# Kernel tuning notes

Hardware: AMD Instinct MI355X
Metric: run time of the kernel (lower is better)

The kernel has to match this reference:

```python
import jax, jax.numpy as jnp
import numpy as np

# Involution2D config (matches init_kwargs)
F = 256          # filters
K = 3            # kernel_size
G = 16           # groups
RR = 4           # reduce_ratio
BN_EPS = 1e-3    # keras BatchNormalization default epsilon


def setup_inputs() -> dict:
    key = jax.random.key(0)
    ks = jax.random.split(key, 8)
    C = 256
    Cr = F // RR                    # reduce_mapping channels = 64
    KKG = K * K * G                 # span_mapping channels = 144
    s = lambda k, sh, fan: jax.random.normal(k, sh, jnp.float32) * (1.0 / np.sqrt(fan))
    return {
        "x": jax.random.normal(ks[0], (4, 128, 128, C), jnp.float32),
        # reduce_mapping: 1x1 conv + BN(inference) + relu
        "Wr": s(ks[1], (C, Cr), C),
        "br": jnp.zeros((Cr,), jnp.float32),
        "gamma": jnp.ones((Cr,), jnp.float32),
        "beta": jnp.zeros((Cr,), jnp.float32),
        "mean": jax.random.normal(ks[2], (Cr,), jnp.float32) * 0.1,
        "var": jax.random.uniform(ks[3], (Cr,), jnp.float32, 0.5, 1.5),
        # span_mapping: 1x1 conv -> K*K*G dynamic weights
        "Ws": s(ks[4], (Cr, KKG), Cr),
        "bs": jnp.zeros((KKG,), jnp.float32),
        # initial_mapping: 1x1 conv -> F (applied since F != K*K*G)
        "Wi": s(ks[5], (C, F), C),
        "bi": jnp.zeros((F,), jnp.float32),
    }


def reference(x, Wr, br, gamma, beta, mean, var, Ws, bs, Wi, bi):
    B, H, W, _ = x.shape
    KK = K * K
    # reduce_mapping: 1x1 conv + BN(inference) + relu
    r = jnp.einsum('bhwc,cd->bhwd', x, Wr) + br
    r = jax.nn.relu((r - mean) * jax.lax.rsqrt(var + BN_EPS) * gamma + beta)
    # span_mapping: per-pixel dynamic kernel weights [B,H,W,KK*G] -> [B,H,W,G,1,KK]
    w = jnp.einsum('bhwd,dk->bhwk', r, Ws) + bs
    w = w.reshape(B, H, W, G, KK)[:, :, :, :, None, :]
    # initial_mapping: 1x1 conv -> F channels
    xi = jnp.einsum('bhwc,cf->bhwf', x, Wi) + bi
    # tf.image.extract_patches (SAME, stride=1, rate=1): layout is
    # (kernel_pos major, channel minor), i.e. flat index = kpos*F + c
    pad = (K - 1) // 2
    xp = jnp.pad(xi, ((0, 0), (pad, pad), (pad, pad), (0, 0)))
    patches = jnp.stack(
        [xp[:, i:i + H, j:j + W, :] for i in range(K) for j in range(K)],
        axis=3)                                   # [B,H,W,KK,F]
    # faithful to the original K.reshape of the flat [KK*F] axis
    patches = patches.reshape(B, H, W, G, F // G, KK)
    out = jnp.sum(w * patches, axis=-1)           # [B,H,W,G,F//G]
    return out.reshape(B, H, W, F)
```

## Files before the change

kernel.cpp:

```cpp
#include <hip/hip_runtime.h>

#define NPIX 65536
#define BN_EPS 1e-3f

typedef __attribute__((ext_vector_type(8))) short bf16x8;
typedef __attribute__((ext_vector_type(4))) float f32x4;

__device__ inline unsigned short f2b(float f) {
    unsigned int u = __float_as_uint(f);
    unsigned int r = (u + 0x7fffu + ((u >> 16) & 1u)) >> 16;
    return (unsigned short)r;
}
__device__ inline float b2f(unsigned short h) {
    return __uint_as_float(((unsigned int)h) << 16);
}

__global__ void k_prep(const float* __restrict__ Wi, const float* __restrict__ Wr,
                       const float* __restrict__ Ws,
                       unsigned short* __restrict__ Bt, unsigned short* __restrict__ Wst) {
    int t = blockIdx.x * 256 + threadIdx.x;
    if (t < 320 * 256) {
        int n = t >> 8, k = t & 255;
        float v = (n < 256) ? Wi[k * 256 + n] : Wr[k * 64 + (n - 256)];
        Bt[t] = f2b(v);
    } else {
        int t2 = t - 320 * 256;
        if (t2 < 144 * 64) {
            int n = t2 >> 6, k = t2 & 63;
            Wst[t2] = f2b(Ws[k * 144 + n]);
        }
    }
}

#define APAD 264
__global__ __launch_bounds__(256, 3) void k1_gemm(
    const float* __restrict__ x, const unsigned short* __restrict__ Bt,
    const float* __restrict__ bi, const float* __restrict__ br,
    const float* __restrict__ gamma, const float* __restrict__ beta,
    const float* __restrict__ mean, const float* __restrict__ var,
    unsigned short* __restrict__ xi_b, unsigned short* __restrict__ r_b)
{
    __shared__ unsigned short As[64 * APAD];
    const int tid = threadIdx.x;
    const int p0 = blockIdx.x * 64;

    {
        const float* xs = x + (long long)p0 * 256;
        for (int i = tid * 4; i < 64 * 256; i += 1024) {
            float4 v = *(const float4*)&xs[i];
            int m = i >> 8, k = i & 255;
            unsigned short* d = &As[m * APAD + k];
            d[0] = f2b(v.x); d[1] = f2b(v.y); d[2] = f2b(v.z); d[3] = f2b(v.w);
        }
    }
    __syncthreads();

    const int wv = tid >> 6;
    const int lane = tid & 63;
    const int col = lane & 15;
    const int quad = lane >> 4;
    const int nt0 = wv * 5;

    f32x4 acc[4][5];
#pragma unroll
    for (int i = 0; i < 4; ++i)
#pragma unroll
        for (int j = 0; j < 5; ++j) acc[i][j] = (f32x4){0.f, 0.f, 0.f, 0.f};

    for (int kc = 0; kc < 8; ++kc) {
        const int kb = kc * 32 + quad * 8;
        bf16x8 a[4], b[5];
#pragma unroll
        for (int mt = 0; mt < 4; ++mt)
            a[mt] = *(const bf16x8*)&As[(mt * 16 + col) * APAD + kb];
#pragma unroll
        for (int nt = 0; nt < 5; ++nt)
            b[nt] = *(const bf16x8*)&Bt[((nt0 + nt) * 16 + col) * 256 + kb];
#pragma unroll
        for (int mt = 0; mt < 4; ++mt)
#pragma unroll
            for (int nt = 0; nt < 5; ++nt)
                acc[mt][nt] = __builtin_amdgcn_mfma_f32_16x16x32_bf16(
                    a[mt], b[nt], acc[mt][nt], 0, 0, 0);
    }

#pragma unroll
    for (int nt = 0; nt < 5; ++nt) {
        const int n = (nt0 + nt) * 16 + col;
        if (n < 256) {
            const float bv = bi[n];
#pragma unroll
            for (int mt = 0; mt < 4; ++mt) {
                const int prow = p0 + mt * 16 + quad * 4;
#pragma unroll
                for (int rg = 0; rg < 4; ++rg)
                    xi_b[(long long)(prow + rg) * 256 + n] = f2b(acc[mt][nt][rg] + bv);
            }
        } else {
            const int d = n - 256;
            const float brd = br[d], md = mean[d], bt = beta[d];
            const float sc = gamma[d] * rsqrtf(var[d] + BN_EPS);
#pragma unroll
            for (int mt = 0; mt < 4; ++mt) {
                const int prow = p0 + mt * 16 + quad * 4;
#pragma unroll
                for (int rg = 0; rg < 4; ++rg) {
                    float v = (acc[mt][nt][rg] + brd - md) * sc + bt;
                    r_b[(long long)(prow + rg) * 64 + d] = f2b(fmaxf(v, 0.f));
                }
            }
        }
    }
}

__global__ __launch_bounds__(256, 4) void k2_span(
    const unsigned short* __restrict__ r_b, const unsigned short* __restrict__ Wst,
    const float* __restrict__ bs, unsigned short* __restrict__ w_b)
{
    const int tid = threadIdx.x;
    const int wv = tid >> 6, lane = tid & 63, col = lane & 15, quad = lane >> 4;
    const int p0 = blockIdx.x * 64 + wv * 16;

    f32x4 acc[9];
#pragma unroll
    for (int i = 0; i < 9; ++i) acc[i] = (f32x4){0.f, 0.f, 0.f, 0.f};

#pragma unroll
    for (int kc = 0; kc < 2; ++kc) {
        const int kb = kc * 32 + quad * 8;
        bf16x8 a = *(const bf16x8*)&r_b[(long long)(p0 + col) * 64 + kb];
        bf16x8 b[9];
#pragma unroll
        for (int nt = 0; nt < 9; ++nt)
            b[nt] = *(const bf16x8*)&Wst[(nt * 16 + col) * 64 + kb];
#pragma unroll
        for (int nt = 0; nt < 9; ++nt)
            acc[nt] = __builtin_amdgcn_mfma_f32_16x16x32_bf16(a, b[nt], acc[nt], 0, 0, 0);
    }
#pragma unroll
    for (int nt = 0; nt < 9; ++nt) {
        const int n = nt * 16 + col;
        const float bv = bs[n];
#pragma unroll
        for (int rg = 0; rg < 4; ++rg)
            w_b[(long long)(p0 + quad * 4 + rg) * 144 + n] = f2b(acc[nt][rg] + bv);
    }
}

#define XROW 264
#define OFF_W (54 * XROW)
#define SM3_TOTAL (54 * XROW + 16 * 144)
__global__ __launch_bounds__(256, 4) void k3_gather(
    const unsigned short* __restrict__ xi_b, const unsigned short* __restrict__ w_b,
    float* __restrict__ out)
{
    __shared__ unsigned short sm[SM3_TOTAL];
    const int tid = threadIdx.x;
    const int pp0 = blockIdx.x * 16;
    const int bb = pp0 >> 14;
    const int h  = (pp0 >> 7) & 127;
    const int w0 = pp0 & 127;

    for (int t = tid; t < 54 * 32; t += 256) {
        const int row = t >> 5, gi = t & 31;
        const int ki = row / 18, kjc = row - ki * 18;
        const int sh = h + ki - 1;
        const int sw = w0 + kjc - 1;
        int4 v = {0, 0, 0, 0};
        if ((unsigned)sh < 128u && (unsigned)sw < 128u)
            v = *(const int4*)&xi_b[(long long)((bb * 128 + sh) * 128 + sw) * 256 + gi * 8];
        *(int4*)&sm[row * XROW + gi * 8] = v;
    }
    for (int t = tid; t < 288; t += 256)
        *(int4*)&sm[OFF_W + t * 8] = *(const int4*)&w_b[(long long)pp0 * 144 + t * 8];
    __syncthreads();

    const int g = tid & 15;
    const int p = tid >> 4;

    const int idx0 = g * 144;
    const int kp0  = idx0 >> 8;
    const int c0   = idx0 & 255;
    int len1 = 256 - c0; if (len1 > 144) len1 = 144;
    const int kp1  = kp0 + 1;
    const int base0 = ((kp0 / 3) * 18 + (kp0 % 3) + p) * XROW + c0;
    const int base1 = (kp1 <= 8) ? (((kp1 / 3) * 18 + (kp1 % 3) + p) * XROW) : 0;

    float wf[9];
#pragma unroll
    for (int kk = 0; kk < 9; ++kk)
        wf[kk] = b2f(sm[OFF_W + p * 144 + g * 9 + kk]);

    float res[16];

    {
        int4 xv[9];
#pragma unroll
        for (int i = 0; i < 9; ++i) {
            const int e = i * 8;
            const int addr = (e < len1) ? (base0 + e) : (base1 + (e - len1));
            xv[i] = *(const int4*)&sm[addr];
        }
#pragma unroll
        for (int f2 = 0; f2 < 8; ++f2) {
            float a = 0.f;
#pragma unroll
            for (int kk = 0; kk < 9; ++kk) {
                const int e = f2 * 9 + kk;
                const int word = ((const int*)&xv[e >> 3])[(e >> 1) & 3];
                const unsigned short u = (e & 1) ? (unsigned short)(((unsigned)word) >> 16)
                                                 : (unsigned short)(word & 0xffff);
                a += wf[kk] * b2f(u);
            }
            res[f2] = a;
        }
    }
    {
        int4 xv[9];
#pragma unroll
        for (int i = 9; i < 18; ++i) {
            const int e = i * 8;
            const int addr = (e < len1) ? (base0 + e) : (base1 + (e - len1));
            xv[i - 9] = *(const int4*)&sm[addr];
        }
#pragma unroll
        for (int f2 = 8; f2 < 16; ++f2) {
            float a = 0.f;
#pragma unroll
            for (int kk = 0; kk < 9; ++kk) {
                const int e = f2 * 9 + kk;
                const int i = (e >> 3) - 9;
                const int word = ((const int*)&xv[i])[(e >> 1) & 3];
                const unsigned short u = (e & 1) ? (unsigned short)(((unsigned)word) >> 16)
                                                 : (unsigned short)(word & 0xffff);
                a += wf[kk] * b2f(u);
            }
            res[f2] = a;
        }
    }

    const long long orow = ((long long)pp0 + p) * 256 + g * 16;
#pragma unroll
    for (int q = 0; q < 4; ++q) {
        float4 o = {res[q * 4 + 0], res[q * 4 + 1], res[q * 4 + 2], res[q * 4 + 3]};
        *(float4*)&out[orow + q * 4] = o;
    }
}

extern "C" void kernel_launch(void* const* d_in, const int* in_sizes, int n_in,
                              void* d_out, int out_size, void* d_ws, size_t ws_size,
                              hipStream_t stream) {
    const float* x     = (const float*)d_in[0];
    const float* Wr    = (const float*)d_in[1];
    const float* br    = (const float*)d_in[2];
    const float* gamma = (const float*)d_in[3];
    const float* beta  = (const float*)d_in[4];
    const float* mean  = (const float*)d_in[5];
    const float* var   = (const float*)d_in[6];
    const float* Ws    = (const float*)d_in[7];
    const float* bs    = (const float*)d_in[8];
    const float* Wi    = (const float*)d_in[9];
    const float* bi    = (const float*)d_in[10];
    float* out = (float*)d_out;

    unsigned char* ws = (unsigned char*)d_ws;
    unsigned short* xi_b = (unsigned short*)(ws + 0);
    unsigned short* r_b  = (unsigned short*)(ws + 33554432);
    unsigned short* w_b  = (unsigned short*)(ws + 41943040);
    unsigned short* Bt   = (unsigned short*)(ws + 60817408);
    unsigned short* Wst  = (unsigned short*)(ws + 60981248);

    k_prep<<<dim3((320 * 256 + 144 * 64 + 255) / 256), dim3(256), 0, stream>>>(
        Wi, Wr, Ws, Bt, Wst);
    k1_gemm<<<dim3(NPIX / 64), dim3(256), 0, stream>>>(
        x, Bt, bi, br, gamma, beta, mean, var, xi_b, r_b);
    k2_span<<<dim3(NPIX / 64), dim3(256), 0, stream>>>(r_b, Wst, bs, w_b);
    k3_gather<<<dim3(NPIX / 16), dim3(256), 0, stream>>>(xi_b, w_b, out);
}
```

Baseline: 206.6 us.

## Fuse span GEMM into reduce GEMM and enlarge gather tiles

Merges the span-mapping GEMM into the first GEMM kernel. The ReLU'd reduce output now stays in shared memory instead of going through global memory, which removes the r_b round-trip and one launch. The first GEMM now handles 32 pixels per block and software-pipelines its B-fragment loads. The gather kernel moves to 32-pixel, 512-thread blocks with a wider halo, which cuts redundant halo loads, and it converts the dynamic weights to fp32 once in LDS. The risks are lower GEMM reuse per block from the smaller M tile, and higher LDS use that may limit occupancy.

```diff
diff --git a/kernel.cpp b/kernel.cpp
--- a/kernel.cpp
+++ b/kernel.cpp
@@ -32,24 +32,26 @@
     }
 }
 
-#define APAD 264
-__global__ __launch_bounds__(256, 3) void k1_gemm(
+#define APAD12 264
+__global__ __launch_bounds__(256, 3) void k12(
     const float* __restrict__ x, const unsigned short* __restrict__ Bt,
     const float* __restrict__ bi, const float* __restrict__ br,
     const float* __restrict__ gamma, const float* __restrict__ beta,
     const float* __restrict__ mean, const float* __restrict__ var,
-    unsigned short* __restrict__ xi_b, unsigned short* __restrict__ r_b)
+    const unsigned short* __restrict__ Wst, const float* __restrict__ bs,
+    unsigned short* __restrict__ xi_b, unsigned short* __restrict__ w_b)
 {
-    __shared__ unsigned short As[64 * APAD];
+    __shared__ unsigned short As[32 * APAD12];
+    __shared__ unsigned short Rs[32 * 72];
     const int tid = threadIdx.x;
-    const int p0 = blockIdx.x * 64;
+    const int p0 = blockIdx.x * 32;
 
     {
         const float* xs = x + (long long)p0 * 256;
-        for (int i = tid * 4; i < 64 * 256; i += 1024) {
+        for (int i = tid * 4; i < 32 * 256; i += 1024) {
             float4 v = *(const float4*)&xs[i];
             int m = i >> 8, k = i & 255;
-            unsigned short* d = &As[m * APAD + k];
+            unsigned short* d = &As[m * APAD12 + k];
             d[0] = f2b(v.x); d[1] = f2b(v.y); d[2] = f2b(v.z); d[3] = f2b(v.w);
         }
     }
@@ -61,27 +63,39 @@
     const int quad = lane >> 4;
     const int nt0 = wv * 5;
 
-    f32x4 acc[4][5];
-#pragma unroll
-    for (int i = 0; i < 4; ++i)
+    f32x4 acc[2][5];
+#pragma unroll
+    for (int i = 0; i < 2; ++i)
 #pragma unroll
         for (int j = 0; j < 5; ++j) acc[i][j] = (f32x4){0.f, 0.f, 0.f, 0.f};
 
+    const unsigned short* bp[5];
+#pragma unroll
+    for (int nt = 0; nt < 5; ++nt)
+        bp[nt] = &Bt[((nt0 + nt) * 16 + col) * 256];
+
+    bf16x8 bc[5];
+#pragma unroll
+    for (int nt = 0; nt < 5; ++nt)
+        bc[nt] = *(const bf16x8*)&bp[nt][quad * 8];
+
+#pragma unroll
     for (int kc = 0; kc < 8; ++kc) {
-        const int kb = kc * 32 + quad * 8;
-        bf16x8 a[4], b[5];
-#pragma unroll
-        for (int mt = 0; mt < 4; ++mt)
-            a[mt] = *(const bf16x8*)&As[(mt * 16 + col) * APAD + kb];
+        const int kb  = kc * 32 + quad * 8;
+        const int kbn = (kc < 7) ? kb + 32 : kb;
+        bf16x8 bn[5];
 #pragma unroll
         for (int nt = 0; nt < 5; ++nt)
-            b[nt] = *(const bf16x8*)&Bt[((nt0 + nt) * 16 + col) * 256 + kb];
-#pragma unroll
-        for (int mt = 0; mt < 4; ++mt)
-#pragma unroll
-            for (int nt = 0; nt < 5; ++nt)
-                acc[mt][nt] = __builtin_amdgcn_mfma_f32_16x16x32_bf16(
-                    a[mt], b[nt], acc[mt][nt], 0, 0, 0);
+            bn[nt] = *(const bf16x8*)&bp[nt][kbn];
+        bf16x8 a0 = *(const bf16x8*)&As[(col) * APAD12 + kb];
+        bf16x8 a1 = *(const bf16x8*)&As[(16 + col) * APAD12 + kb];
+#pragma unroll
+        for (int nt = 0; nt < 5; ++nt) {
+            acc[0][nt] = __builtin_amdgcn_mfma_f32_16x16x32_bf16(a0, bc[nt], acc[0][nt], 0, 0, 0);
+            acc[1][nt] = __builtin_amdgcn_mfma_f32_16x16x32_bf16(a1, bc[nt], acc[1][nt], 0, 0, 0);
+        }
+#pragma unroll
+        for (int nt = 0; nt < 5; ++nt) bc[nt] = bn[nt];
     }
 
 #pragma unroll
@@ -90,7 +104,7 @@
         if (n < 256) {
             const float bv = bi[n];
 #pragma unroll
-            for (int mt = 0; mt < 4; ++mt) {
+            for (int mt = 0; mt < 2; ++mt) {
                 const int prow = p0 + mt * 16 + quad * 4;
 #pragma unroll
                 for (int rg = 0; rg < 4; ++rg)
@@ -101,78 +115,86 @@
             const float brd = br[d], md = mean[d], bt = beta[d];
             const float sc = gamma[d] * rsqrtf(var[d] + BN_EPS);
 #pragma unroll
-            for (int mt = 0; mt < 4; ++mt) {
-                const int prow = p0 + mt * 16 + quad * 4;
+            for (int mt = 0; mt < 2; ++mt) {
+                const int mrow = mt * 16 + quad * 4;
 #pragma unroll
                 for (int rg = 0; rg < 4; ++rg) {
                     float v = (acc[mt][nt][rg] + brd - md) * sc + bt;
-                    r_b[(long long)(prow + rg) * 64 + d] = f2b(fmaxf(v, 0.f));
+                    Rs[(mrow + rg) * 72 + d] = f2b(fmaxf(v, 0.f));
                 }
             }
         }
     }
-}
-
-__global__ __launch_bounds__(256, 4) void k2_span(
-    const unsigned short* __restrict__ r_b, const unsigned short* __restrict__ Wst,
-    const float* __restrict__ bs, unsigned short* __restrict__ w_b)
-{
-    const int tid = threadIdx.x;
-    const int wv = tid >> 6, lane = tid & 63, col = lane & 15, quad = lane >> 4;
-    const int p0 = blockIdx.x * 64 + wv * 16;
-
-    f32x4 acc[9];
-#pragma unroll
-    for (int i = 0; i < 9; ++i) acc[i] = (f32x4){0.f, 0.f, 0.f, 0.f};
-
-#pragma unroll
-    for (int kc = 0; kc < 2; ++kc) {
-        const int kb = kc * 32 + quad * 8;
-        bf16x8 a = *(const bf16x8*)&r_b[(long long)(p0 + col) * 64 + kb];
-        bf16x8 b[9];
-#pragma unroll
-        for (int nt = 0; nt < 9; ++nt)
-            b[nt] = *(const bf16x8*)&Wst[(nt * 16 + col) * 64 + kb];
-#pragma unroll
-        for (int nt = 0; nt < 9; ++nt)
-            acc[nt] = __builtin_amdgcn_mfma_f32_16x16x32_bf16(a, b[nt], acc[nt], 0, 0, 0);
-    }
-#pragma unroll
-    for (int nt = 0; nt < 9; ++nt) {
-        const int n = nt * 16 + col;
-        const float bv = bs[n];
-#pragma unroll
-        for (int rg = 0; rg < 4; ++rg)
-            w_b[(long long)(p0 + quad * 4 + rg) * 144 + n] = f2b(acc[nt][rg] + bv);
-    }
-}
-
-#define XROW 264
-#define OFF_W (54 * XROW)
-#define SM3_TOTAL (54 * XROW + 16 * 144)
-__global__ __launch_bounds__(256, 4) void k3_gather(
+    __syncthreads();
+
+    {
+        const int mt_w = wv & 1;
+        const int jn0  = (wv >> 1) ? 5 : 0;
+        const int jcnt = (wv >> 1) ? 4 : 5;
+        f32x4 wacc[5];
+#pragma unroll
+        for (int j = 0; j < 5; ++j) wacc[j] = (f32x4){0.f, 0.f, 0.f, 0.f};
+#pragma unroll
+        for (int kc = 0; kc < 2; ++kc) {
+            const int kb = kc * 32 + quad * 8;
+            bf16x8 ra = *(const bf16x8*)&Rs[(mt_w * 16 + col) * 72 + kb];
+#pragma unroll
+            for (int j = 0; j < 5; ++j) {
+                if (j < jcnt) {
+                    bf16x8 wb = *(const bf16x8*)&Wst[((jn0 + j) * 16 + col) * 64 + kb];
+                    wacc[j] = __builtin_amdgcn_mfma_f32_16x16x32_bf16(ra, wb, wacc[j], 0, 0, 0);
+                }
+            }
+        }
+#pragma unroll
+        for (int j = 0; j < 5; ++j) {
+            if (j < jcnt) {
+                const int n = (jn0 + j) * 16 + col;
+                const float bv = bs[n];
+#pragma unroll
+                for (int rg = 0; rg < 4; ++rg)
+                    w_b[(long long)(p0 + mt_w * 16 + quad * 4 + rg) * 144 + n] =
+                        f2b(wacc[j][rg] + bv);
+            }
+        }
+    }
+}
+
+#define XR3 264
+#define NROW3 102
+__global__ __launch_bounds__(512, 4) void k3_gather(
     const unsigned short* __restrict__ xi_b, const unsigned short* __restrict__ w_b,
     float* __restrict__ out)
 {
-    __shared__ unsigned short sm[SM3_TOTAL];
+    __shared__ unsigned short smx[NROW3 * XR3];
+    __shared__ float smw[32 * 148];
     const int tid = threadIdx.x;
-    const int pp0 = blockIdx.x * 16;
+    const int pp0 = blockIdx.x * 32;
     const int bb = pp0 >> 14;
     const int h  = (pp0 >> 7) & 127;
     const int w0 = pp0 & 127;
 
-    for (int t = tid; t < 54 * 32; t += 256) {
-        const int row = t >> 5, gi = t & 31;
-        const int ki = row / 18, kjc = row - ki * 18;
-        const int sh = h + ki - 1;
-        const int sw = w0 + kjc - 1;
-        int4 v = {0, 0, 0, 0};
-        if ((unsigned)sh < 128u && (unsigned)sw < 128u)
-            v = *(const int4*)&xi_b[(long long)((bb * 128 + sh) * 128 + sw) * 256 + gi * 8];
-        *(int4*)&sm[row * XROW + gi * 8] = v;
-    }
-    for (int t = tid; t < 288; t += 256)
-        *(int4*)&sm[OFF_W + t * 8] = *(const int4*)&w_b[(long long)pp0 * 144 + t * 8];
+    for (int t = tid; t < NROW3 * 32 + 576; t += 512) {
+        if (t < NROW3 * 32) {
+            const int row = t >> 5, gi = t & 31;
+            const int ki = row / 34, kjc = row - ki * 34;
+            const int sh = h + ki - 1;
+            const int sw = w0 + kjc - 1;
+            int4 v = {0, 0, 0, 0};
+            if ((unsigned)sh < 128u && (unsigned)sw < 128u)
+                v = *(const int4*)&xi_b[(long long)((bb * 128 + sh) * 128 + sw) * 256 + gi * 8];
+            *(int4*)&smx[row * XR3 + gi * 8] = v;
+        } else {
+            const int t2 = t - NROW3 * 32;
+            const int p = t2 / 18, rem = t2 - p * 18;
+            const int n0 = rem * 8;
+            int4 v = *(const int4*)&w_b[((long long)(pp0 + p)) * 144 + n0];
+            const unsigned short* u = (const unsigned short*)&v;
+            float* d = &smw[p * 148 + n0];
+#pragma unroll
+            for (int i = 0; i < 8; ++i) d[i] = b2f(u[i]);
+        }
+    }
     __syncthreads();
 
     const int g = tid & 15;
@@ -183,13 +205,13 @@
     const int c0   = idx0 & 255;
     int len1 = 256 - c0; if (len1 > 144) len1 = 144;
     const int kp1  = kp0 + 1;
-    const int base0 = ((kp0 / 3) * 18 + (kp0 % 3) + p) * XROW + c0;
-    const int base1 = (kp1 <= 8) ? (((kp1 / 3) * 18 + (kp1 % 3) + p) * XROW) : 0;
+    const int base0 = ((kp0 / 3) * 34 + (kp0 % 3) + p) * XR3 + c0;
+    const int base1 = (kp1 <= 8) ? (((kp1 / 3) * 34 + (kp1 % 3) + p) * XR3) : 0;
 
     float wf[9];
 #pragma unroll
     for (int kk = 0; kk < 9; ++kk)
-        wf[kk] = b2f(sm[OFF_W + p * 144 + g * 9 + kk]);
+        wf[kk] = smw[p * 148 + g * 9 + kk];
 
     float res[16];
 
@@ -199,7 +221,7 @@
         for (int i = 0; i < 9; ++i) {
             const int e = i * 8;
             const int addr = (e < len1) ? (base0 + e) : (base1 + (e - len1));
-            xv[i] = *(const int4*)&sm[addr];
+            xv[i] = *(const int4*)&smx[addr];
         }
 #pragma unroll
         for (int f2 = 0; f2 < 8; ++f2) {
@@ -221,7 +243,7 @@
         for (int i = 9; i < 18; ++i) {
             const int e = i * 8;
             const int addr = (e < len1) ? (base0 + e) : (base1 + (e - len1));
-            xv[i - 9] = *(const int4*)&sm[addr];
+            xv[i - 9] = *(const int4*)&smx[addr];
         }
 #pragma unroll
         for (int f2 = 8; f2 < 16; ++f2) {
@@ -265,15 +287,12 @@
 
     unsigned char* ws = (unsigned char*)d_ws;
     unsigned short* xi_b = (unsigned short*)(ws + 0);
-    unsigned short* r_b  = (unsigned short*)(ws + 33554432);
-    unsigned short* w_b  = (unsigned short*)(ws + 41943040);
-    unsigned short* Bt   = (unsigned short*)(ws + 60817408);
-    unsigned short* Wst  = (unsigned short*)(ws + 60981248);
-
-    k_prep<<<dim3((320 * 256 + 144 * 64 + 255) / 256), dim3(256), 0, stream>>>(
-        Wi, Wr, Ws, Bt, Wst);
-    k1_gemm<<<dim3(NPIX / 64), dim3(256), 0, stream>>>(
-        x, Bt, bi, br, gamma, beta, mean, var, xi_b, r_b);
-    k2_span<<<dim3(NPIX / 64), dim3(256), 0, stream>>>(r_b, Wst, bs, w_b);
-    k3_gather<<<dim3(NPIX / 16), dim3(256), 0, stream>>>(xi_b, w_b, out);
-}
+    unsigned short* w_b  = (unsigned short*)(ws + 33554432);
+    unsigned short* Bt   = (unsigned short*)(ws + 52428800);
+    unsigned short* Wst  = (unsigned short*)(ws + 52592640);
+
+    k_prep<<<dim3(356), dim3(256), 0, stream>>>(Wi, Wr, Ws, Bt, Wst);
+    k12<<<dim3(NPIX / 32), dim3(256), 0, stream>>>(
+        x, Bt, bi, br, gamma, beta, mean, var, Wst, bs, xi_b, w_b);
+    k3_gather<<<dim3(NPIX / 32), dim3(512), 0, stream>>>(xi_b, w_b, out);
+}
```

Result: slower. 216.4 us (+4.7%).

## Fuse pointwise GEMMs, span mapping and involution gather into one tiled kernel

Applied to the files above, without the earlier changes.

Replaces the three-kernel pipeline (1x1 GEMMs, span GEMM, gather) with one kernel per 8x16 spatial tile. The kernel recomputes the xi and reduce projections for the 10x18 haloed tile in shared memory, keeps the B weights in registers, and prefetches the next x chunk while the MFMAs run. This removes the global round-trips of the intermediate xi, r and w tensors. The cost is halo recomputation (180 rows for 128 output pixels), large register and LDS use, and only 512 blocks.

```diff
diff --git a/kernel.cpp b/kernel.cpp
--- a/kernel.cpp
+++ b/kernel.cpp
@@ -1,6 +1,5 @@
 #include <hip/hip_runtime.h>
 
-#define NPIX 65536
 #define BN_EPS 1e-3f
 
 typedef __attribute__((ext_vector_type(8))) short bf16x8;
@@ -32,218 +31,276 @@
     }
 }
 
-#define APAD 264
-__global__ __launch_bounds__(256, 3) void k1_gemm(
+#define XIP 264
+#define RS_OFF (180 * XIP)
+#define RSP 72
+#define WL_OFF (RS_OFF + 180 * RSP)
+#define SMN (WL_OFF + 128 * 144)
+
+__global__ __launch_bounds__(512, 2) void k_fused(
     const float* __restrict__ x, const unsigned short* __restrict__ Bt,
+    const unsigned short* __restrict__ Wst,
     const float* __restrict__ bi, const float* __restrict__ br,
     const float* __restrict__ gamma, const float* __restrict__ beta,
     const float* __restrict__ mean, const float* __restrict__ var,
-    unsigned short* __restrict__ xi_b, unsigned short* __restrict__ r_b)
+    const float* __restrict__ bs, float* __restrict__ out)
 {
-    __shared__ unsigned short As[64 * APAD];
+    __shared__ __attribute__((aligned(16))) unsigned short sm[SMN];
     const int tid = threadIdx.x;
-    const int p0 = blockIdx.x * 64;
-
-    {
-        const float* xs = x + (long long)p0 * 256;
-        for (int i = tid * 4; i < 64 * 256; i += 1024) {
-            float4 v = *(const float4*)&xs[i];
-            int m = i >> 8, k = i & 255;
-            unsigned short* d = &As[m * APAD + k];
-            d[0] = f2b(v.x); d[1] = f2b(v.y); d[2] = f2b(v.z); d[3] = f2b(v.w);
-        }
-    }
-    __syncthreads();
+    const int bx = blockIdx.x;
+    const int w0 = (bx & 7) * 16;
+    const int h0 = ((bx >> 3) & 15) * 8;
+    const int bb = bx >> 7;
 
     const int wv = tid >> 6;
     const int lane = tid & 63;
     const int col = lane & 15;
     const int quad = lane >> 4;
-    const int nt0 = wv * 5;
-
-    f32x4 acc[4][5];
-#pragma unroll
-    for (int i = 0; i < 4; ++i)
-#pragma unroll
-        for (int j = 0; j < 5; ++j) acc[i][j] = (f32x4){0.f, 0.f, 0.f, 0.f};
-
-    for (int kc = 0; kc < 8; ++kc) {
-        const int kb = kc * 32 + quad * 8;
-        bf16x8 a[4], b[5];
-#pragma unroll
-        for (int mt = 0; mt < 4; ++mt)
-            a[mt] = *(const bf16x8*)&As[(mt * 16 + col) * APAD + kb];
-#pragma unroll
-        for (int nt = 0; nt < 5; ++nt)
-            b[nt] = *(const bf16x8*)&Bt[((nt0 + nt) * 16 + col) * 256 + kb];
-#pragma unroll
-        for (int mt = 0; mt < 4; ++mt)
-#pragma unroll
-            for (int nt = 0; nt < 5; ++nt)
-                acc[mt][nt] = __builtin_amdgcn_mfma_f32_16x16x32_bf16(
-                    a[mt], b[nt], acc[mt][nt], 0, 0, 0);
-    }
-
-#pragma unroll
-    for (int nt = 0; nt < 5; ++nt) {
-        const int n = (nt0 + nt) * 16 + col;
-        if (n < 256) {
-            const float bv = bi[n];
-#pragma unroll
-            for (int mt = 0; mt < 4; ++mt) {
-                const int prow = p0 + mt * 16 + quad * 4;
-#pragma unroll
-                for (int rg = 0; rg < 4; ++rg)
-                    xi_b[(long long)(prow + rg) * 256 + n] = f2b(acc[mt][nt][rg] + bv);
-            }
+
+    const float bi_v0 = bi[(2 * wv) * 16 + col];
+    const float bi_v1 = bi[(2 * wv + 1) * 16 + col];
+    const int dcl = (wv & 3) * 16 + col;
+    const float brd = br[dcl];
+    const float md  = mean[dcl];
+    const float sc  = gamma[dcl] * rsqrtf(var[dcl] + BN_EPS);
+    const float btv = beta[dcl];
+
+    bf16x8 bx0[8], bx1[8], brr[8];
+    {
+        const unsigned short* p0 = &Bt[((2 * wv) * 16 + col) * 256];
+        const unsigned short* p1 = &Bt[((2 * wv + 1) * 16 + col) * 256];
+#pragma unroll
+        for (int kc = 0; kc < 8; ++kc) {
+            bx0[kc] = *(const bf16x8*)&p0[kc * 32 + quad * 8];
+            bx1[kc] = *(const bf16x8*)&p1[kc * 32 + quad * 8];
+        }
+        if (wv < 4) {
+            const unsigned short* pr = &Bt[((16 + wv) * 16 + col) * 256];
+#pragma unroll
+            for (int kc = 0; kc < 8; ++kc)
+                brr[kc] = *(const bf16x8*)&pr[kc * 32 + quad * 8];
+        }
+    }
+
+    const int chq = (tid & 15) * 4;
+
+    float4 vcur[4];
+    int hp_cur;
+    {
+        hp_cur = (tid >> 4);
+        int r = hp_cur / 18, cc = hp_cur - r * 18;
+        int gh = h0 - 1 + r, gw = w0 - 1 + cc;
+        bool ok = (hp_cur < 180) && ((unsigned)gh < 128u) && ((unsigned)gw < 128u);
+        if (ok) {
+            const float* src = x + (((long long)(bb * 128 + gh)) * 128 + gw) * 256 + chq;
+#pragma unroll
+            for (int j = 0; j < 4; ++j) vcur[j] = *(const float4*)&src[j * 64];
         } else {
-            const int d = n - 256;
-            const float brd = br[d], md = mean[d], bt = beta[d];
-            const float sc = gamma[d] * rsqrtf(var[d] + BN_EPS);
-#pragma unroll
-            for (int mt = 0; mt < 4; ++mt) {
-                const int prow = p0 + mt * 16 + quad * 4;
+#pragma unroll
+            for (int j = 0; j < 4; ++j) vcur[j] = (float4){0.f, 0.f, 0.f, 0.f};
+        }
+        if (hp_cur < 180) {
+#pragma unroll
+            for (int j = 0; j < 4; ++j) {
+                uint2 pk;
+                pk.x = (unsigned)f2b(vcur[j].x) | ((unsigned)f2b(vcur[j].y) << 16);
+                pk.y = (unsigned)f2b(vcur[j].z) | ((unsigned)f2b(vcur[j].w) << 16);
+                *(uint2*)&sm[hp_cur * XIP + chq + j * 64] = pk;
+            }
+        }
+    }
+    __syncthreads();
+
+    for (int c = 0; c < 6; ++c) {
+        float4 vn[4];
+        int hp_n = 192;
+        if (c < 5) {
+            hp_n = (c + 1) * 32 + (tid >> 4);
+            int r = hp_n / 18, cc = hp_n - r * 18;
+            int gh = h0 - 1 + r, gw = w0 - 1 + cc;
+            bool ok = (hp_n < 180) && ((unsigned)gh < 128u) && ((unsigned)gw < 128u);
+            if (ok) {
+                const float* src = x + (((long long)(bb * 128 + gh)) * 128 + gw) * 256 + chq;
+#pragma unroll
+                for (int j = 0; j < 4; ++j) vn[j] = *(const float4*)&src[j * 64];
+            } else {
+#pragma unroll
+                for (int j = 0; j < 4; ++j) vn[j] = (float4){0.f, 0.f, 0.f, 0.f};
+            }
+        }
+
+        f32x4 a00 = {0.f,0.f,0.f,0.f}, a01 = a00, a10 = a00, a11 = a00;
+        f32x4 ar0 = a00, ar1 = a00;
+        {
+            const int rowA0 = (c * 32 + col) * XIP;
+            const int rowA1 = (c * 32 + 16 + col) * XIP;
+#pragma unroll
+            for (int kc = 0; kc < 8; ++kc) {
+                const int kb = kc * 32 + quad * 8;
+                bf16x8 a0 = *(const bf16x8*)&sm[rowA0 + kb];
+                bf16x8 a1 = *(const bf16x8*)&sm[rowA1 + kb];
+                a00 = __builtin_amdgcn_mfma_f32_16x16x32_bf16(a0, bx0[kc], a00, 0, 0, 0);
+                a10 = __builtin_amdgcn_mfma_f32_16x16x32_bf16(a1, bx0[kc], a10, 0, 0, 0);
+                a01 = __builtin_amdgcn_mfma_f32_16x16x32_bf16(a0, bx1[kc], a01, 0, 0, 0);
+                a11 = __builtin_amdgcn_mfma_f32_16x16x32_bf16(a1, bx1[kc], a11, 0, 0, 0);
+                if (wv < 4) {
+                    ar0 = __builtin_amdgcn_mfma_f32_16x16x32_bf16(a0, brr[kc], ar0, 0, 0, 0);
+                    ar1 = __builtin_amdgcn_mfma_f32_16x16x32_bf16(a1, brr[kc], ar1, 0, 0, 0);
+                }
+            }
+        }
+        __syncthreads();
+
+        if (c < 5 && hp_n < 180) {
+#pragma unroll
+            for (int j = 0; j < 4; ++j) {
+                uint2 pk;
+                pk.x = (unsigned)f2b(vn[j].x) | ((unsigned)f2b(vn[j].y) << 16);
+                pk.y = (unsigned)f2b(vn[j].z) | ((unsigned)f2b(vn[j].w) << 16);
+                *(uint2*)&sm[hp_n * XIP + chq + j * 64] = pk;
+            }
+        }
+
+        {
+            const int n0 = (2 * wv) * 16 + col;
+            const int n1 = (2 * wv + 1) * 16 + col;
+            const int rb = c * 32 + quad * 4;
+#pragma unroll
+            for (int rg = 0; rg < 4; ++rg) {
+                const int r0 = rb + rg, r1 = rb + 16 + rg;
+                if (r0 < 180) {
+                    sm[r0 * XIP + n0] = f2b(a00[rg] + bi_v0);
+                    sm[r0 * XIP + n1] = f2b(a01[rg] + bi_v1);
+                }
+                if (r1 < 180) {
+                    sm[r1 * XIP + n0] = f2b(a10[rg] + bi_v0);
+                    sm[r1 * XIP + n1] = f2b(a11[rg] + bi_v1);
+                }
+            }
+            if (wv < 4) {
 #pragma unroll
                 for (int rg = 0; rg < 4; ++rg) {
-                    float v = (acc[mt][nt][rg] + brd - md) * sc + bt;
-                    r_b[(long long)(prow + rg) * 64 + d] = f2b(fmaxf(v, 0.f));
-                }
-            }
-        }
-    }
-}
-
-__global__ __launch_bounds__(256, 4) void k2_span(
-    const unsigned short* __restrict__ r_b, const unsigned short* __restrict__ Wst,
-    const float* __restrict__ bs, unsigned short* __restrict__ w_b)
-{
-    const int tid = threadIdx.x;
-    const int wv = tid >> 6, lane = tid & 63, col = lane & 15, quad = lane >> 4;
-    const int p0 = blockIdx.x * 64 + wv * 16;
-
-    f32x4 acc[9];
-#pragma unroll
-    for (int i = 0; i < 9; ++i) acc[i] = (f32x4){0.f, 0.f, 0.f, 0.f};
-
-#pragma unroll
-    for (int kc = 0; kc < 2; ++kc) {
-        const int kb = kc * 32 + quad * 8;
-        bf16x8 a = *(const bf16x8*)&r_b[(long long)(p0 + col) * 64 + kb];
-        bf16x8 b[9];
-#pragma unroll
-        for (int nt = 0; nt < 9; ++nt)
-            b[nt] = *(const bf16x8*)&Wst[(nt * 16 + col) * 64 + kb];
-#pragma unroll
-        for (int nt = 0; nt < 9; ++nt)
-            acc[nt] = __builtin_amdgcn_mfma_f32_16x16x32_bf16(a, b[nt], acc[nt], 0, 0, 0);
-    }
-#pragma unroll
-    for (int nt = 0; nt < 9; ++nt) {
-        const int n = nt * 16 + col;
-        const float bv = bs[n];
-#pragma unroll
-        for (int rg = 0; rg < 4; ++rg)
-            w_b[(long long)(p0 + quad * 4 + rg) * 144 + n] = f2b(acc[nt][rg] + bv);
-    }
-}
-
-#define XROW 264
-#define OFF_W (54 * XROW)
-#define SM3_TOTAL (54 * XROW + 16 * 144)
-__global__ __launch_bounds__(256, 4) void k3_gather(
-    const unsigned short* __restrict__ xi_b, const unsigned short* __restrict__ w_b,
-    float* __restrict__ out)
-{
-    __shared__ unsigned short sm[SM3_TOTAL];
-    const int tid = threadIdx.x;
-    const int pp0 = blockIdx.x * 16;
-    const int bb = pp0 >> 14;
-    const int h  = (pp0 >> 7) & 127;
-    const int w0 = pp0 & 127;
-
-    for (int t = tid; t < 54 * 32; t += 256) {
-        const int row = t >> 5, gi = t & 31;
-        const int ki = row / 18, kjc = row - ki * 18;
-        const int sh = h + ki - 1;
-        const int sw = w0 + kjc - 1;
-        int4 v = {0, 0, 0, 0};
-        if ((unsigned)sh < 128u && (unsigned)sw < 128u)
-            v = *(const int4*)&xi_b[(long long)((bb * 128 + sh) * 128 + sw) * 256 + gi * 8];
-        *(int4*)&sm[row * XROW + gi * 8] = v;
-    }
-    for (int t = tid; t < 288; t += 256)
-        *(int4*)&sm[OFF_W + t * 8] = *(const int4*)&w_b[(long long)pp0 * 144 + t * 8];
+                    const int r0 = rb + rg, r1 = rb + 16 + rg;
+                    if (r0 < 180) {
+                        float v = (ar0[rg] + brd - md) * sc + btv;
+                        sm[RS_OFF + r0 * RSP + dcl] = f2b(fmaxf(v, 0.f));
+                    }
+                    if (r1 < 180) {
+                        float v = (ar1[rg] + brd - md) * sc + btv;
+                        sm[RS_OFF + r1 * RSP + dcl] = f2b(fmaxf(v, 0.f));
+                    }
+                }
+            }
+        }
+        __syncthreads();
+    }
+
+    {
+        f32x4 wacc[9];
+#pragma unroll
+        for (int j = 0; j < 9; ++j) wacc[j] = (f32x4){0.f, 0.f, 0.f, 0.f};
+        const int arow = (19 + wv * 18 + col) * RSP;
+#pragma unroll
+        for (int kc = 0; kc < 2; ++kc) {
+            const int kb = kc * 32 + quad * 8;
+            bf16x8 ra = *(const bf16x8*)&sm[RS_OFF + arow + kb];
+#pragma unroll
+            for (int j = 0; j < 9; ++j) {
+                bf16x8 wb = *(const bf16x8*)&Wst[(j * 16 + col) * 64 + kb];
+                wacc[j] = __builtin_amdgcn_mfma_f32_16x16x32_bf16(ra, wb, wacc[j], 0, 0, 0);
+            }
+        }
+#pragma unroll
+        for (int j = 0; j < 9; ++j) {
+            const int n = j * 16 + col;
+            const float bv = bs[n];
+            const int prow = wv * 16 + quad * 4;
+#pragma unroll
+            for (int rg = 0; rg < 4; ++rg)
+                sm[WL_OFF + (prow + rg) * 144 + n] = f2b(wacc[j][rg] + bv);
+        }
+    }
     __syncthreads();
 
-    const int g = tid & 15;
-    const int p = tid >> 4;
-
-    const int idx0 = g * 144;
-    const int kp0  = idx0 >> 8;
-    const int c0   = idx0 & 255;
-    int len1 = 256 - c0; if (len1 > 144) len1 = 144;
-    const int kp1  = kp0 + 1;
-    const int base0 = ((kp0 / 3) * 18 + (kp0 % 3) + p) * XROW + c0;
-    const int base1 = (kp1 <= 8) ? (((kp1 / 3) * 18 + (kp1 % 3) + p) * XROW) : 0;
-
-    float wf[9];
-#pragma unroll
-    for (int kk = 0; kk < 9; ++kk)
-        wf[kk] = b2f(sm[OFF_W + p * 144 + g * 9 + kk]);
-
-    float res[16];
-
     {
-        int4 xv[9];
-#pragma unroll
-        for (int i = 0; i < 9; ++i) {
-            const int e = i * 8;
-            const int addr = (e < len1) ? (base0 + e) : (base1 + (e - len1));
-            xv[i] = *(const int4*)&sm[addr];
-        }
-#pragma unroll
-        for (int f2 = 0; f2 < 8; ++f2) {
-            float a = 0.f;
-#pragma unroll
-            for (int kk = 0; kk < 9; ++kk) {
-                const int e = f2 * 9 + kk;
-                const int word = ((const int*)&xv[e >> 3])[(e >> 1) & 3];
-                const unsigned short u = (e & 1) ? (unsigned short)(((unsigned)word) >> 16)
-                                                 : (unsigned short)(word & 0xffff);
-                a += wf[kk] * b2f(u);
-            }
-            res[f2] = a;
-        }
-    }
-    {
-        int4 xv[9];
-#pragma unroll
-        for (int i = 9; i < 18; ++i) {
-            const int e = i * 8;
-            const int addr = (e < len1) ? (base0 + e) : (base1 + (e - len1));
-            xv[i - 9] = *(const int4*)&sm[addr];
-        }
-#pragma unroll
-        for (int f2 = 8; f2 < 16; ++f2) {
-            float a = 0.f;
-#pragma unroll
-            for (int kk = 0; kk < 9; ++kk) {
-                const int e = f2 * 9 + kk;
-                const int i = (e >> 3) - 9;
-                const int word = ((const int*)&xv[i])[(e >> 1) & 3];
-                const unsigned short u = (e & 1) ? (unsigned short)(((unsigned)word) >> 16)
-                                                 : (unsigned short)(word & 0xffff);
-                a += wf[kk] * b2f(u);
-            }
-            res[f2] = a;
-        }
-    }
-
-    const long long orow = ((long long)pp0 + p) * 256 + g * 16;
-#pragma unroll
-    for (int q = 0; q < 4; ++q) {
-        float4 o = {res[q * 4 + 0], res[q * 4 + 1], res[q * 4 + 2], res[q * 4 + 3]};
-        *(float4*)&out[orow + q * 4] = o;
+        const int g = tid & 15;
+        const int pb = tid >> 4;
+
+        const int idx0 = g * 144;
+        const int kp0  = idx0 >> 8;
+        const int c0   = idx0 & 255;
+        int len1 = 256 - c0; if (len1 > 144) len1 = 144;
+        const int kp1  = kp0 + 1;
+        const int koff0 = (kp0 / 3) * 18 + (kp0 % 3);
+        const int koff1 = (kp1 <= 8) ? ((kp1 / 3) * 18 + (kp1 % 3)) : 0;
+
+#pragma unroll
+        for (int jj = 0; jj < 4; ++jj) {
+            const int p = pb + 32 * jj;
+            const int phb = (p >> 4) * 18 + (p & 15);
+            const int base0 = (phb + koff0) * XIP + c0;
+            const int base1 = (phb + koff1) * XIP;
+
+            float wf[9];
+#pragma unroll
+            for (int kk = 0; kk < 9; ++kk)
+                wf[kk] = b2f(sm[WL_OFF + p * 144 + g * 9 + kk]);
+
+            float res[16];
+            {
+                int4 xv[9];
+#pragma unroll
+                for (int i = 0; i < 9; ++i) {
+                    const int e = i * 8;
+                    const int addr = (e < len1) ? (base0 + e) : (base1 + (e - len1));
+                    xv[i] = *(const int4*)&sm[addr];
+                }
+#pragma unroll
+                for (int f2 = 0; f2 < 8; ++f2) {
+                    float a = 0.f;
+#pragma unroll
+                    for (int kk = 0; kk < 9; ++kk) {
+                        const int e = f2 * 9 + kk;
+                        const int word = ((const int*)&xv[e >> 3])[(e >> 1) & 3];
+                        const unsigned short u = (e & 1) ? (unsigned short)(((unsigned)word) >> 16)
+                                                         : (unsigned short)(word & 0xffff);
+                        a += wf[kk] * b2f(u);
+                    }
+                    res[f2] = a;
+                }
+            }
+            {
+                int4 xv[9];
+#pragma unroll
+                for (int i = 9; i < 18; ++i) {
+                    const int e = i * 8;
+                    const int addr = (e < len1) ? (base0 + e) : (base1 + (e - len1));
+                    xv[i - 9] = *(const int4*)&sm[addr];
+                }
+#pragma unroll
+                for (int f2 = 8; f2 < 16; ++f2) {
+                    float a = 0.f;
+#pragma unroll
+                    for (int kk = 0; kk < 9; ++kk) {
+                        const int e = f2 * 9 + kk;
+                        const int i = (e >> 3) - 9;
+                        const int word = ((const int*)&xv[i])[(e >> 1) & 3];
+                        const unsigned short u = (e & 1) ? (unsigned short)(((unsigned)word) >> 16)
+                                                         : (unsigned short)(word & 0xffff);
+                        a += wf[kk] * b2f(u);
+                    }
+                    res[f2] = a;
+                }
+            }
+
+            const long long orow =
+                (((long long)(bb * 128 + h0 + (p >> 4))) * 128 + (w0 + (p & 15))) * 256 + g * 16;
+#pragma unroll
+            for (int q = 0; q < 4; ++q) {
+                float4 o = {res[q * 4 + 0], res[q * 4 + 1], res[q * 4 + 2], res[q * 4 + 3]};
+                *(float4*)&out[orow + q * 4] = o;
+            }
+        }
     }
 }
 
@@ -264,16 +321,10 @@
     float* out = (float*)d_out;
 
     unsigned char* ws = (unsigned char*)d_ws;
-    unsigned short* xi_b = (unsigned short*)(ws + 0);
-    unsigned short* r_b  = (unsigned short*)(ws + 33554432);
-    unsigned short* w_b  = (unsigned short*)(ws + 41943040);
-    unsigned short* Bt   = (unsigned short*)(ws + 60817408);
-    unsigned short* Wst  = (unsigned short*)(ws + 60981248);
-
-    k_prep<<<dim3((320 * 256 + 144 * 64 + 255) / 256), dim3(256), 0, stream>>>(
-        Wi, Wr, Ws, Bt, Wst);
-    k1_gemm<<<dim3(NPIX / 64), dim3(256), 0, stream>>>(
-        x, Bt, bi, br, gamma, beta, mean, var, xi_b, r_b);
-    k2_span<<<dim3(NPIX / 64), dim3(256), 0, stream>>>(r_b, Wst, bs, w_b);
-    k3_gather<<<dim3(NPIX / 16), dim3(256), 0, stream>>>(xi_b, w_b, out);
-}
+    unsigned short* Bt  = (unsigned short*)(ws + 0);
+    unsigned short* Wst = (unsigned short*)(ws + 163840);
+
+    k_prep<<<dim3(356), dim3(256), 0, stream>>>(Wi, Wr, Ws, Bt, Wst);
+    k_fused<<<dim3(512), dim3(512), 0, stream>>>(
+        x, Bt, Wst, bi, br, gamma, beta, mean, var, bs, out);
+}
```

New measurement: 172.7 us. 1.2x faster.
